# Kernel optimization log

Hardware: AMD Instinct MI355X
Metric: run time of the kernel (lower is better)

## Reference

```python
import jax, jax.numpy as jnp
import numpy as np

NUM_HEADS = 16
CLAMP = 1e4


def setup_inputs() -> dict:
    key = jax.random.key(0)
    ks = jax.random.split(key, 8)
    B, Nq, Nkv, Cq, Ckv = 4, 2048, 2048, 1024, 768
    s_q = 1.0 / np.sqrt(Cq)
    s_kv = 1.0 / np.sqrt(Ckv)
    return {
        "query": jax.random.normal(ks[0], (B, Nq, Cq), jnp.float32),
        "key_value": jax.random.normal(ks[1], (B, Nkv, Ckv), jnp.float32),
        "Wq": jax.random.normal(ks[2], (Cq, Cq), jnp.float32) * s_q,
        "bq": jnp.zeros((Cq,), jnp.float32),
        "Wk": jax.random.normal(ks[3], (Ckv, Cq), jnp.float32) * s_kv,
        "bk": jnp.zeros((Cq,), jnp.float32),
        "Wv": jax.random.normal(ks[4], (Ckv, Cq), jnp.float32) * s_kv,
        "bv": jnp.zeros((Cq,), jnp.float32),
        "Wo": jax.random.normal(ks[5], (Cq, Cq), jnp.float32) * s_q,
        "bo": jnp.zeros((Cq,), jnp.float32),
    }


def reference(query, key_value, Wq, bq, Wk, bk, Wv, bv, Wo, bo):
    B, Nq, Cq = query.shape
    Nkv = key_value.shape[1]
    H = NUM_HEADS
    D = Cq // H
    scale = D ** (-0.5)

    # projections -> [B, H, N, D]
    q = (query @ Wq + bq).reshape(B, Nq, H, D).transpose(0, 2, 1, 3)
    k = (key_value @ Wk + bk).reshape(B, Nkv, H, D).transpose(0, 2, 1, 3)
    v = (key_value @ Wv + bv).reshape(B, Nkv, H, D).transpose(0, 2, 1, 3)

    # scores [B, H, Nq, Nkv] with clamp (mask=None path)
    attn = jnp.einsum("bhqd,bhkd->bhqk", q, k) * scale
    attn = jnp.clip(attn, -CLAMP, CLAMP)
    attn = jax.nn.softmax(attn, axis=-1)
    # NaN fallback: replace with uniform attention if any NaN present
    attn = jnp.where(jnp.any(jnp.isnan(attn)),
                     jnp.asarray(1.0 / Nkv, attn.dtype), attn)

    # weighted sum -> [B, Nq, Cq]
    x = jnp.einsum("bhqk,bhkd->bqhd", attn, v).reshape(B, Nq, Cq)
    return x @ Wo + bo
```

## Files before the change

kernel.cpp:

```cpp
#include <hip/hip_runtime.h>
#include <hip/hip_bf16.h>
#include <stdint.h>


typedef unsigned short u16;
typedef __attribute__((ext_vector_type(4))) short bf16x4;
typedef __attribute__((ext_vector_type(8))) short bf16x8;
typedef __attribute__((ext_vector_type(4))) float f32x4;
typedef __attribute__((ext_vector_type(16))) float f32x16;

__device__ __forceinline__ u16 f2bf(float x) {
  union { float f; uint32_t u; } c; c.f = x;
  uint32_t r = c.u + 0x7fffu + ((c.u >> 16) & 1u);
  return (u16)(r >> 16);
}

__device__ __forceinline__ uint32_t pkbf(float a, float b) {
#if __has_builtin(__builtin_amdgcn_cvt_pk_bf16_f32)
  typedef __attribute__((ext_vector_type(2))) __bf16 bf2;
  bf2 r = __builtin_amdgcn_cvt_pk_bf16_f32(a, b);
  return __builtin_bit_cast(uint32_t, r);
#else
  return (uint32_t)f2bf(a) | ((uint32_t)f2bf(b) << 16);
#endif
}

__device__ __forceinline__ void gld16(const void* g, void* l) {
  __builtin_amdgcn_global_load_lds(
      (const __attribute__((address_space(1))) void*)g,
      (__attribute__((address_space(3))) void*)l, 16, 0, 0);
}

__global__ void cvt_f32_bf16(const float* __restrict__ in, u16* __restrict__ out, int n) {
  int i = (blockIdx.x * 256 + threadIdx.x) * 8;
  if (i >= n) return;
  float4 a = *(const float4*)(in + i);
  float4 b = *(const float4*)(in + i + 4);
  union { u16 u[8]; uint4 v; } o;
  o.u[0] = f2bf(a.x); o.u[1] = f2bf(a.y); o.u[2] = f2bf(a.z); o.u[3] = f2bf(a.w);
  o.u[4] = f2bf(b.x); o.u[5] = f2bf(b.y); o.u[6] = f2bf(b.z); o.u[7] = f2bf(b.w);
  *(uint4*)(out + i) = o.v;
}

__global__ void transpose_cvt(const float* __restrict__ in, u16* __restrict__ out,
                              int R, int C) {
  __shared__ float tile[64][65];
  int c0 = blockIdx.x * 64, r0 = blockIdx.y * 64;
  #pragma unroll
  for (int it = 0; it < 16; it++) {
    int idx = threadIdx.x + it * 256;
    int lr = idx >> 6, lc = idx & 63;
    tile[lr][lc] = in[(size_t)(r0 + lr) * C + c0 + lc];
  }
  __syncthreads();
  #pragma unroll
  for (int it = 0; it < 16; it++) {
    int idx = threadIdx.x + it * 256;
    int lc = idx >> 6, lr = idx & 63;
    out[(size_t)(c0 + lc) * R + r0 + lr] = f2bf(tile[lr][lc]);
  }
}

template<int MODE>
__global__ __launch_bounds__(256, 2)
void gemm_bt(const u16* __restrict__ A, const u16* __restrict__ BT,
             const float* __restrict__ bias, void* __restrict__ Cout,
             int M, int N, int K, float scale) {
  __shared__ u16 As[128 * 32];
  __shared__ u16 Bs[128 * 32];
  const int tid = threadIdx.x;
  const int w = tid >> 6, l = tid & 63;
  const int lm = l & 15, lq = l >> 4;
  const int m0 = blockIdx.y * 128, n0 = blockIdx.x * 128;
  const int wr = w >> 1, wc = w & 1;
  f32x4 acc[4][4] = {};
  const int rsw = (lq ^ ((lm >> 1) & 3)) * 8;

  for (int k0 = 0; k0 < K; k0 += 32) {
    #pragma unroll
    for (int rep = 0; rep < 2; rep++) {
      int g = w * 128 + rep * 64 + l;
      int row = g >> 2;
      int kc = (g & 3) ^ ((row >> 1) & 3);
      gld16(A + (size_t)(m0 + row) * K + k0 + kc * 8, &As[g * 8]);
      gld16(BT + (size_t)(n0 + row) * K + k0 + kc * 8, &Bs[g * 8]);
    }
    __syncthreads();
    bf16x8 af[4], bf[4];
    #pragma unroll
    for (int i = 0; i < 4; i++)
      af[i] = *(const bf16x8*)&As[(wr * 64 + i * 16 + lm) * 32 + rsw];
    #pragma unroll
    for (int j = 0; j < 4; j++)
      bf[j] = *(const bf16x8*)&Bs[(wc * 64 + j * 16 + lm) * 32 + rsw];
    #pragma unroll
    for (int i = 0; i < 4; i++)
      #pragma unroll
      for (int j = 0; j < 4; j++)
        acc[i][j] = __builtin_amdgcn_mfma_f32_16x16x32_bf16(af[i], bf[j], acc[i][j], 0, 0, 0);
    __syncthreads();
  }

  #pragma unroll
  for (int j = 0; j < 4; j++) {
    int gn = n0 + wc * 64 + j * 16 + lm;
    float bi = bias[gn];
    #pragma unroll
    for (int i = 0; i < 4; i++) {
      int gm = m0 + wr * 64 + i * 16 + lq * 4;
      #pragma unroll
      for (int r = 0; r < 4; r++) {
        float val = (acc[i][j][r] + bi) * scale;
        if (MODE == 0) {
          ((float*)Cout)[(size_t)(gm + r) * N + gn] = val;
        } else if (MODE == 1) {
          ((u16*)Cout)[(size_t)(gm + r) * N + gn] = f2bf(val);
        } else {
          int row = gm + r;
          int bb = row >> 11, nn = row & 2047;
          ((u16*)Cout)[((size_t)bb * N + gn) * 2048 + nn] = f2bf(val);
        }
      }
    }
  }
}

__global__ __launch_bounds__(256, 3)
void attn_kernel(const u16* __restrict__ Q, const u16* __restrict__ Kb,
                 const u16* __restrict__ Vt, u16* __restrict__ X) {
  __shared__ u16 Ks[2][4096];
  __shared__ u16 Vs[2][4096];
  const int tid = threadIdx.x, w = tid >> 6, l = tid & 63;
  const int l31 = l & 31, h5 = l >> 5;
  const int bh = blockIdx.x, b = bh >> 4, h = bh & 15;
  const int q0 = blockIdx.y * 128 + w * 32;

  const u16* Kg = Kb + (size_t)b * 2048 * 1024 + h * 64;
  const u16* Vg = Vt + (size_t)bh * 64 * 2048;

  #pragma unroll
  for (int is = 0; is < 2; is++) {
    int s = is * 256 + tid;
    int r = s >> 3, c = (s & 7) ^ (r & 7);
    gld16(Kg + (size_t)r * 1024 + c * 8, &Ks[0][s * 8]);
    gld16(Vg + (size_t)r * 2048 + c * 8, &Vs[0][s * 8]);
  }

  bf16x8 qf[4];
  const u16* qp = Q + ((size_t)(b * 2048 + q0 + l31)) * 1024 + h * 64 + h5 * 8;
  #pragma unroll
  for (int t = 0; t < 4; t++) qf[t] = *(const bf16x8*)(qp + t * 16);

  f32x16 xacc[2] = {};
  float lsum = 0.f;

  __syncthreads();

  for (int it = 0; it < 32; it++) {
    const int cur = it & 1;
    if (it < 31) {
      const int n1 = (it + 1) * 64;
      #pragma unroll
      for (int is = 0; is < 2; is++) {
        int s = is * 256 + tid;
        int r = s >> 3, c = (s & 7) ^ (r & 7);
        gld16(Kg + (size_t)(n1 + r) * 1024 + c * 8, &Ks[cur ^ 1][s * 8]);
        gld16(Vg + (size_t)r * 2048 + n1 + c * 8, &Vs[cur ^ 1][s * 8]);
      }
    }
    const u16* kb = Ks[cur];
    const u16* vb = Vs[cur];

    #pragma unroll
    for (int sub = 0; sub < 2; sub++) {
      f32x16 st = {};
      const int r = sub * 32 + l31, rx = r & 7;
      #pragma unroll
      for (int t = 0; t < 4; t++) {
        bf16x8 kf = *(const bf16x8*)&kb[(r * 8 + (((t << 1) + h5) ^ rx)) * 8];
        st = __builtin_amdgcn_mfma_f32_32x32x16_bf16(kf, qf[t], st, 0, 0, 0);
      }
      #pragma unroll
      for (int u = 0; u < 4; u++) {
        float p0 = __builtin_amdgcn_exp2f(st[4 * u + 0]);
        float p1 = __builtin_amdgcn_exp2f(st[4 * u + 1]);
        float p2 = __builtin_amdgcn_exp2f(st[4 * u + 2]);
        float p3 = __builtin_amdgcn_exp2f(st[4 * u + 3]);
        lsum += (p0 + p1) + (p2 + p3);
        union { uint32_t q[2]; bf16x4 v; } pk_;
        pk_.q[0] = pkbf(p0, p1);
        pk_.q[1] = pkbf(p2, p3);
        const int c = sub * 4 + u;
        #pragma unroll
        for (int dt = 0; dt < 2; dt++) {
          const int vr = dt * 32 + l31;
          bf16x4 vf = *(const bf16x4*)&vb[(vr * 8 + (c ^ (vr & 7))) * 8 + h5 * 4];
          xacc[dt] = __builtin_amdgcn_mfma_f32_32x32x8bf16_1k(vf, pk_.v, xacc[dt], 0, 0, 0);
        }
      }
    }
    __syncthreads();
  }

  const float inv = 1.0f / (lsum + __shfl_xor(lsum, 32));
  u16* xp = X + ((size_t)(b * 2048 + q0 + l31)) * 1024 + h * 64;
  #pragma unroll
  for (int dt = 0; dt < 2; dt++)
    #pragma unroll
    for (int g = 0; g < 4; g++) {
      const int d0 = dt * 32 + g * 8 + h5 * 4;
      uint2 o;
      o.x = pkbf(xacc[dt][4 * g + 0] * inv, xacc[dt][4 * g + 1] * inv);
      o.y = pkbf(xacc[dt][4 * g + 2] * inv, xacc[dt][4 * g + 3] * inv);
      *(uint2*)(xp + d0) = o;
    }
}

extern "C" void kernel_launch(void* const* d_in, const int* in_sizes, int n_in,
                              void* d_out, int out_size, void* d_ws, size_t ws_size,
                              hipStream_t stream) {
  const float* query     = (const float*)d_in[0];
  const float* key_value = (const float*)d_in[1];
  const float* Wq = (const float*)d_in[2];
  const float* bq = (const float*)d_in[3];
  const float* Wk = (const float*)d_in[4];
  const float* bk = (const float*)d_in[5];
  const float* Wv = (const float*)d_in[6];
  const float* bv = (const float*)d_in[7];
  const float* Wo = (const float*)d_in[8];
  const float* bo = (const float*)d_in[9];
  float* out = (float*)d_out;

  char* ws = (char*)d_ws;
  size_t off = 0;
  auto alloc = [&](size_t bytes) -> void* {
    void* p = ws + off; off += (bytes + 255) & ~(size_t)255; return p;
  };
  u16* qb  = (u16*)alloc((size_t)8192 * 1024 * 2);
  u16* kvb = (u16*)alloc((size_t)8192 * 768 * 2);
  u16* WqT = (u16*)alloc((size_t)1024 * 1024 * 2);
  u16* WkT = (u16*)alloc((size_t)1024 * 768 * 2);
  u16* WvT = (u16*)alloc((size_t)1024 * 768 * 2);
  u16* WoT = (u16*)alloc((size_t)1024 * 1024 * 2);
  u16* Qb  = (u16*)alloc((size_t)8192 * 1024 * 2);
  u16* Kbf = (u16*)alloc((size_t)8192 * 1024 * 2);
  u16* Vt  = (u16*)alloc((size_t)8192 * 1024 * 2);
  u16* Xb  = (u16*)alloc((size_t)8192 * 1024 * 2);

  cvt_f32_bf16<<<(8192 * 1024) / 2048, 256, 0, stream>>>(query, qb, 8192 * 1024);
  cvt_f32_bf16<<<(8192 * 768) / 2048, 256, 0, stream>>>(key_value, kvb, 8192 * 768);
  transpose_cvt<<<dim3(1024 / 64, 1024 / 64), 256, 0, stream>>>(Wq, WqT, 1024, 1024);
  transpose_cvt<<<dim3(1024 / 64, 768 / 64), 256, 0, stream>>>(Wk, WkT, 768, 1024);
  transpose_cvt<<<dim3(1024 / 64, 768 / 64), 256, 0, stream>>>(Wv, WvT, 768, 1024);
  transpose_cvt<<<dim3(1024 / 64, 1024 / 64), 256, 0, stream>>>(Wo, WoT, 1024, 1024);

  const float qscale = 0.125f * 1.4426950408889634f;
  gemm_bt<1><<<dim3(8, 64), 256, 0, stream>>>(qb, WqT, bq, Qb, 8192, 1024, 1024, qscale);
  gemm_bt<1><<<dim3(8, 64), 256, 0, stream>>>(kvb, WkT, bk, Kbf, 8192, 1024, 768, 1.0f);
  gemm_bt<2><<<dim3(8, 64), 256, 0, stream>>>(kvb, WvT, bv, Vt, 8192, 1024, 768, 1.0f);

  attn_kernel<<<dim3(64, 16), 256, 0, stream>>>(Qb, Kbf, Vt, Xb);

  gemm_bt<0><<<dim3(8, 64), 256, 0, stream>>>(Xb, WoT, bo, out, 8192, 1024, 1024, 1.0f);
}
```

Before: 336.6 us.

## Deepen GEMM K-tile, stage epilogue through LDS, and streamline attention addressing

The GEMM K step per barrier goes from 32 to 64, using a single byte-addressed LDS buffer with XOR swizzle and precomputed pointers. The bf16 epilogues are staged through per-wave LDS tiles so global stores are coalesced 16-byte writes. In MODE 1 the MFMA operands are swapped so each lane holds contiguous columns and can load the bias as a float4. The attention kernel precomputes its load pointers and LDS offsets, splits the row sum across four accumulators, unrolls the loop by two and raises the occupancy hint to 4, which risks register pressure.

```diff
diff --git a/kernel.cpp b/kernel.cpp
--- a/kernel.cpp
+++ b/kernel.cpp
@@ -66,118 +66,184 @@
 void gemm_bt(const u16* __restrict__ A, const u16* __restrict__ BT,
              const float* __restrict__ bias, void* __restrict__ Cout,
              int M, int N, int K, float scale) {
-  __shared__ u16 As[128 * 32];
-  __shared__ u16 Bs[128 * 32];
+  __shared__ __align__(16) char smem[36864];
   const int tid = threadIdx.x;
   const int w = tid >> 6, l = tid & 63;
   const int lm = l & 15, lq = l >> 4;
   const int m0 = blockIdx.y * 128, n0 = blockIdx.x * 128;
   const int wr = w >> 1, wc = w & 1;
   f32x4 acc[4][4] = {};
-  const int rsw = (lq ^ ((lm >> 1) & 3)) * 8;
-
-  for (int k0 = 0; k0 < K; k0 += 32) {
-    #pragma unroll
-    for (int rep = 0; rep < 2; rep++) {
-      int g = w * 128 + rep * 64 + l;
-      int row = g >> 2;
-      int kc = (g & 3) ^ ((row >> 1) & 3);
-      gld16(A + (size_t)(m0 + row) * K + k0 + kc * 8, &As[g * 8]);
-      gld16(BT + (size_t)(n0 + row) * K + k0 + kc * 8, &Bs[g * 8]);
+
+  const u16* ap[4]; const u16* bp[4]; int ldA[4], ldB[4];
+  #pragma unroll
+  for (int it2 = 0; it2 < 4; it2++) {
+    int s = it2 * 256 + tid;
+    int row = s >> 3, cl = (s & 7) ^ (row & 7);
+    ap[it2] = A + (size_t)(m0 + row) * K + cl * 8;
+    bp[it2] = BT + (size_t)(n0 + row) * K + cl * 8;
+    ldA[it2] = s * 16;
+    ldB[it2] = 16384 + s * 16;
+  }
+  int abase[4], bbase[4];
+  #pragma unroll
+  for (int i = 0; i < 4; i++) {
+    int m = wr * 64 + i * 16 + lm;
+    abase[i] = m * 128 + ((lq ^ (m & 7)) << 4);
+    int n = wc * 64 + i * 16 + lm;
+    bbase[i] = 16384 + n * 128 + ((lq ^ (n & 7)) << 4);
+  }
+
+  for (int k0 = 0; k0 < K; k0 += 64) {
+    #pragma unroll
+    for (int it2 = 0; it2 < 4; it2++) {
+      gld16(ap[it2], smem + ldA[it2]);
+      gld16(bp[it2], smem + ldB[it2]);
+      ap[it2] += 64; bp[it2] += 64;
     }
     __syncthreads();
-    bf16x8 af[4], bf[4];
-    #pragma unroll
-    for (int i = 0; i < 4; i++)
-      af[i] = *(const bf16x8*)&As[(wr * 64 + i * 16 + lm) * 32 + rsw];
-    #pragma unroll
-    for (int j = 0; j < 4; j++)
-      bf[j] = *(const bf16x8*)&Bs[(wc * 64 + j * 16 + lm) * 32 + rsw];
-    #pragma unroll
-    for (int i = 0; i < 4; i++)
+    #pragma unroll
+    for (int kk = 0; kk < 2; kk++) {
+      bf16x8 af[4], bf[4];
+      #pragma unroll
+      for (int i = 0; i < 4; i++)
+        af[i] = *(const bf16x8*)(smem + (abase[i] ^ (kk << 6)));
       #pragma unroll
       for (int j = 0; j < 4; j++)
-        acc[i][j] = __builtin_amdgcn_mfma_f32_16x16x32_bf16(af[i], bf[j], acc[i][j], 0, 0, 0);
+        bf[j] = *(const bf16x8*)(smem + (bbase[j] ^ (kk << 6)));
+      #pragma unroll
+      for (int i = 0; i < 4; i++)
+        #pragma unroll
+        for (int j = 0; j < 4; j++) {
+          if (MODE == 1)
+            acc[i][j] = __builtin_amdgcn_mfma_f32_16x16x32_bf16(bf[j], af[i], acc[i][j], 0, 0, 0);
+          else
+            acc[i][j] = __builtin_amdgcn_mfma_f32_16x16x32_bf16(af[i], bf[j], acc[i][j], 0, 0, 0);
+        }
+    }
     __syncthreads();
   }
 
-  #pragma unroll
-  for (int j = 0; j < 4; j++) {
-    int gn = n0 + wc * 64 + j * 16 + lm;
-    float bi = bias[gn];
-    #pragma unroll
-    for (int i = 0; i < 4; i++) {
-      int gm = m0 + wr * 64 + i * 16 + lq * 4;
-      #pragma unroll
-      for (int r = 0; r < 4; r++) {
-        float val = (acc[i][j][r] + bi) * scale;
-        if (MODE == 0) {
-          ((float*)Cout)[(size_t)(gm + r) * N + gn] = val;
-        } else if (MODE == 1) {
-          ((u16*)Cout)[(size_t)(gm + r) * N + gn] = f2bf(val);
-        } else {
-          int row = gm + r;
-          int bb = row >> 11, nn = row & 2047;
-          ((u16*)Cout)[((size_t)bb * N + gn) * 2048 + nn] = f2bf(val);
-        }
-      }
-    }
-  }
-}
-
-__global__ __launch_bounds__(256, 3)
+  if (MODE == 0) {
+    #pragma unroll
+    for (int j = 0; j < 4; j++) {
+      int gn = n0 + wc * 64 + j * 16 + lm;
+      float bi = bias[gn];
+      #pragma unroll
+      for (int i = 0; i < 4; i++) {
+        int gm = m0 + wr * 64 + i * 16 + lq * 4;
+        #pragma unroll
+        for (int r = 0; r < 4; r++)
+          ((float*)Cout)[(size_t)(gm + r) * N + gn] = (acc[i][j][r] + bi) * scale;
+      }
+    }
+    return;
+  }
+
+  u16* etile = (u16*)(smem + w * 9216);
+  const int xr = l >> 3, cc = (l & 7) ^ xr;
+
+  if (MODE == 1) {
+    #pragma unroll
+    for (int j = 0; j < 4; j++) {
+      float4 b4 = *(const float4*)&bias[n0 + wc * 64 + j * 16 + lq * 4];
+      #pragma unroll
+      for (int i = 0; i < 4; i++) {
+        uint2 pkd;
+        pkd.x = pkbf((acc[i][j][0] + b4.x) * scale, (acc[i][j][1] + b4.y) * scale);
+        pkd.y = pkbf((acc[i][j][2] + b4.z) * scale, (acc[i][j][3] + b4.w) * scale);
+        *(uint2*)&etile[(i * 16 + lm) * 72 + j * 16 + lq * 4] = pkd;
+      }
+    }
+    u16* gbase = (u16*)Cout + (size_t)(m0 + wr * 64) * N + n0 + wc * 64;
+    #pragma unroll
+    for (int co = 0; co < 8; co++) {
+      int ml = co * 8 + xr;
+      uint4 d = *(const uint4*)&etile[ml * 72 + cc * 8];
+      *(uint4*)&gbase[(size_t)ml * N + cc * 8] = d;
+    }
+  } else {
+    #pragma unroll
+    for (int j = 0; j < 4; j++) {
+      float bi = bias[n0 + wc * 64 + j * 16 + lm];
+      #pragma unroll
+      for (int i = 0; i < 4; i++) {
+        uint2 pkd;
+        pkd.x = pkbf(acc[i][j][0] + bi, acc[i][j][1] + bi);
+        pkd.y = pkbf(acc[i][j][2] + bi, acc[i][j][3] + bi);
+        *(uint2*)&etile[(j * 16 + lm) * 72 + i * 16 + lq * 4] = pkd;
+      }
+    }
+    const int bb = m0 >> 11, mloc = (m0 & 2047) + wr * 64;
+    u16* gbase = (u16*)Cout + ((size_t)bb * N + n0 + wc * 64) * 2048 + mloc;
+    #pragma unroll
+    for (int co = 0; co < 8; co++) {
+      int dl = co * 8 + xr;
+      uint4 d = *(const uint4*)&etile[dl * 72 + cc * 8];
+      *(uint4*)&gbase[(size_t)dl * 2048 + cc * 8] = d;
+    }
+  }
+}
+
+__global__ __launch_bounds__(256, 4)
 void attn_kernel(const u16* __restrict__ Q, const u16* __restrict__ Kb,
                  const u16* __restrict__ Vt, u16* __restrict__ X) {
-  __shared__ u16 Ks[2][4096];
-  __shared__ u16 Vs[2][4096];
+  __shared__ __align__(16) char smem[32768];
   const int tid = threadIdx.x, w = tid >> 6, l = tid & 63;
   const int l31 = l & 31, h5 = l >> 5;
   const int bh = blockIdx.x, b = bh >> 4, h = bh & 15;
   const int q0 = blockIdx.y * 128 + w * 32;
+  const int rx = l31 & 7;
 
   const u16* Kg = Kb + (size_t)b * 2048 * 1024 + h * 64;
   const u16* Vg = Vt + (size_t)bh * 64 * 2048;
 
-  #pragma unroll
-  for (int is = 0; is < 2; is++) {
-    int s = is * 256 + tid;
-    int r = s >> 3, c = (s & 7) ^ (r & 7);
-    gld16(Kg + (size_t)r * 1024 + c * 8, &Ks[0][s * 8]);
-    gld16(Vg + (size_t)r * 2048 + c * 8, &Vs[0][s * 8]);
-  }
+  const u16 *kp0, *kp1, *vp0, *vp1;
+  {
+    int s = tid, r = s >> 3, c = (s & 7) ^ (r & 7);
+    kp0 = Kg + (size_t)r * 1024 + c * 8;
+    vp0 = Vg + (size_t)r * 2048 + c * 8;
+    s = 256 + tid; r = s >> 3; c = (s & 7) ^ (r & 7);
+    kp1 = Kg + (size_t)r * 1024 + c * 8;
+    vp1 = Vg + (size_t)r * 2048 + c * 8;
+  }
+  const int kd0 = tid * 16, kd1 = (256 + tid) * 16;
 
   bf16x8 qf[4];
-  const u16* qp = Q + ((size_t)(b * 2048 + q0 + l31)) * 1024 + h * 64 + h5 * 8;
-  #pragma unroll
-  for (int t = 0; t < 4; t++) qf[t] = *(const bf16x8*)(qp + t * 16);
+  {
+    const u16* qp = Q + ((size_t)(b * 2048 + q0 + l31)) * 1024 + h * 64 + h5 * 8;
+    #pragma unroll
+    for (int t = 0; t < 4; t++) qf[t] = *(const bf16x8*)(qp + t * 16);
+  }
+
+  const int kvb_ = (l31 << 7) | ((rx ^ h5) << 4);
+  const int vbase_ = 16384 | (l31 << 7) | (rx << 4) | (h5 << 3);
 
   f32x16 xacc[2] = {};
-  float lsum = 0.f;
-
+  f32x4 ls4 = {0.f, 0.f, 0.f, 0.f};
+  const f32x16 KZ = {};
+
+  gld16(kp0, smem + kd0); gld16(kp1, smem + kd1);
+  gld16(vp0, smem + 16384 + kd0); gld16(vp1, smem + 16384 + kd1);
+  kp0 += 65536; kp1 += 65536; vp0 += 64; vp1 += 64;
   __syncthreads();
 
+  #pragma unroll 2
   for (int it = 0; it < 32; it++) {
     const int cur = it & 1;
     if (it < 31) {
-      const int n1 = (it + 1) * 64;
-      #pragma unroll
-      for (int is = 0; is < 2; is++) {
-        int s = is * 256 + tid;
-        int r = s >> 3, c = (s & 7) ^ (r & 7);
-        gld16(Kg + (size_t)(n1 + r) * 1024 + c * 8, &Ks[cur ^ 1][s * 8]);
-        gld16(Vg + (size_t)r * 2048 + n1 + c * 8, &Vs[cur ^ 1][s * 8]);
-      }
-    }
-    const u16* kb = Ks[cur];
-    const u16* vb = Vs[cur];
-
+      const int nb = (cur ^ 1) << 13;
+      gld16(kp0, smem + nb + kd0); gld16(kp1, smem + nb + kd1);
+      gld16(vp0, smem + 16384 + nb + kd0); gld16(vp1, smem + 16384 + nb + kd1);
+      kp0 += 65536; kp1 += 65536; vp0 += 64; vp1 += 64;
+    }
     #pragma unroll
     for (int sub = 0; sub < 2; sub++) {
-      f32x16 st = {};
-      const int r = sub * 32 + l31, rx = r & 7;
-      #pragma unroll
-      for (int t = 0; t < 4; t++) {
-        bf16x8 kf = *(const bf16x8*)&kb[(r * 8 + (((t << 1) + h5) ^ rx)) * 8];
+      const int km = (cur << 13) | (sub << 12);
+      bf16x8 kf = *(const bf16x8*)(smem + (kvb_ ^ (km | (0 << 5))));
+      f32x16 st = __builtin_amdgcn_mfma_f32_32x32x16_bf16(kf, qf[0], KZ, 0, 0, 0);
+      #pragma unroll
+      for (int t = 1; t < 4; t++) {
+        kf = *(const bf16x8*)(smem + (kvb_ ^ (km | (t << 5))));
         st = __builtin_amdgcn_mfma_f32_32x32x16_bf16(kf, qf[t], st, 0, 0, 0);
       }
       #pragma unroll
@@ -186,15 +252,14 @@
         float p1 = __builtin_amdgcn_exp2f(st[4 * u + 1]);
         float p2 = __builtin_amdgcn_exp2f(st[4 * u + 2]);
         float p3 = __builtin_amdgcn_exp2f(st[4 * u + 3]);
-        lsum += (p0 + p1) + (p2 + p3);
+        ls4[u] += (p0 + p1) + (p2 + p3);
         union { uint32_t q[2]; bf16x4 v; } pk_;
         pk_.q[0] = pkbf(p0, p1);
         pk_.q[1] = pkbf(p2, p3);
         const int c = sub * 4 + u;
         #pragma unroll
         for (int dt = 0; dt < 2; dt++) {
-          const int vr = dt * 32 + l31;
-          bf16x4 vf = *(const bf16x4*)&vb[(vr * 8 + (c ^ (vr & 7))) * 8 + h5 * 4];
+          bf16x4 vf = *(const bf16x4*)(smem + (vbase_ ^ ((cur << 13) | (dt << 12) | (c << 4))));
           xacc[dt] = __builtin_amdgcn_mfma_f32_32x32x8bf16_1k(vf, pk_.v, xacc[dt], 0, 0, 0);
         }
       }
@@ -202,6 +267,7 @@
     __syncthreads();
   }
 
+  float lsum = (ls4[0] + ls4[1]) + (ls4[2] + ls4[3]);
   const float inv = 1.0f / (lsum + __shfl_xor(lsum, 32));
   u16* xp = X + ((size_t)(b * 2048 + q0 + l31)) * 1024 + h * 64;
   #pragma unroll
```

After: 342.4 us. Within noise of the previous version (+1.7%).
